# Performance work log

Measured on AMD Instinct MI355X. Metric: run time of the kernel, lower is better.

## Reference

```python
import jax, jax.numpy as jnp
import numpy as np

POOL = 7                     # cfg.POOLING_SIZE
PRE = 2 * POOL               # pre_pool_size (max_pool=True path)
LEVEL_HW = (256, 128, 64, 32)  # square H=W of P2..P5 for a 1024x1024 image


def setup_inputs() -> dict:
    key = jax.random.key(0)
    ks = jax.random.split(key, 8)
    C = 256
    feats = {f"p{i + 2}": jax.random.normal(ks[i], (1, C, s, s), dtype=jnp.float32)
             for i, s in enumerate(LEVEL_HW)}
    N = 1000
    IMG = 1024.0
    x1 = jax.random.uniform(ks[4], (N,), minval=0.0, maxval=IMG - 33.0)
    y1 = jax.random.uniform(ks[5], (N,), minval=0.0, maxval=IMG - 33.0)
    w = jax.random.uniform(ks[6], (N,), minval=32.0, maxval=512.0)
    h = jax.random.uniform(ks[7], (N,), minval=32.0, maxval=512.0)
    x2 = jnp.minimum(x1 + w, IMG - 1.0)
    y2 = jnp.minimum(y1 + h, IMG - 1.0)
    rois = jnp.stack([jnp.zeros((N,), jnp.float32), x1, y1, x2, y2], axis=1)
    inp = dict(feats)
    inp["rois"] = rois
    return inp


def _crop_pool_fpn(p2, p3, p4, p5, rois):
    """Faithful vectorized version of Network._crop_pool_layer_fpn (max_pool=True).

    Per-ROI FPN level select, affine-grid + bilinear grid_sample
    (align_corners=True semantics, zeros padding), then 2x2 max pool.
    """
    levels = (p2, p3, p4, p5)
    C = p2.shape[1]
    Hm = p2.shape[2]  # largest (P2) map; all levels padded up to this
    # Pad every level into one [L, Hm, Wm, C] array (NHWC for clean gathers).
    feats = jnp.stack([
        jnp.pad(jnp.transpose(f[0], (1, 2, 0)),
                ((0, Hm - f.shape[2]), (0, Hm - f.shape[3]), (0, 0)))
        for f in levels])

    x1, y1, x2, y2 = rois[:, 1], rois[:, 2], rois[:, 3], rois[:, 4]
    w = jnp.where(x2 - x1 <= 0, 1e-14, x2 - x1)
    h = jnp.where(y2 - y1 <= 0, 1e-14, y2 - y1)
    kf = 4.0 + jnp.log2(jnp.sqrt(w * h) / 224.0)   # k0 + log2(sqrt(wh)/224)
    kf = jnp.clip(kf, 2.0, 5.0)                     # clamp BEFORE round (as in source)
    k = jnp.round(kf)
    scale = 2.0 ** k
    lvl = k.astype(jnp.int32) - 2                   # [N] in [0,4)
    x1s, y1s, x2s, y2s = x1 / scale, y1 / scale, x2 / scale, y2 / scale

    # affine_grid(theta) + align_corners=True grid_sample collapses to direct
    # pixel coords: px = (x1+x2)/2 + t*(x2-x1)/2, t = linspace(-1, 1, PRE).
    t = jnp.linspace(-1.0, 1.0, PRE)
    px = (x1s + x2s)[:, None] * 0.5 + t[None, :] * ((x2s - x1s)[:, None] * 0.5)  # [N,PRE]
    py = (y1s + y2s)[:, None] * 0.5 + t[None, :] * ((y2s - y1s)[:, None] * 0.5)
    PX = jnp.broadcast_to(px[:, None, :], (px.shape[0], PRE, PRE))  # [N,PRE,PRE]
    PY = jnp.broadcast_to(py[:, :, None], (py.shape[0], PRE, PRE))

    HWl = jnp.asarray(LEVEL_HW, jnp.float32)[lvl][:, None, None]  # per-ROI level size (square)
    x0 = jnp.floor(PX)
    y0 = jnp.floor(PY)
    dx = PX - x0
    dy = PY - y0

    def gather(yi, xi):
        inb = ((xi >= 0) & (xi < HWl) & (yi >= 0) & (yi < HWl)).astype(feats.dtype)
        yc = jnp.clip(yi, 0, Hm - 1).astype(jnp.int32)
        xc = jnp.clip(xi, 0, Hm - 1).astype(jnp.int32)
        v = feats[lvl[:, None, None], yc, xc]      # [N,PRE,PRE,C]
        return v * inb[..., None]                   # zeros padding

    out = (gather(y0, x0) * ((1 - dy) * (1 - dx))[..., None]
           + gather(y0, x0 + 1) * ((1 - dy) * dx)[..., None]
           + gather(y0 + 1, x0) * (dy * (1 - dx))[..., None]
           + gather(y0 + 1, x0 + 1) * (dy * dx)[..., None])  # [N,PRE,PRE,C]

    crops = jnp.transpose(out, (0, 3, 1, 2))        # [N,C,PRE,PRE]
    N = crops.shape[0]
    crops = crops.reshape(N, C, POOL, 2, POOL, 2).max(axis=(3, 5))  # 2x2 max pool
    return crops                                     # [N,C,POOL,POOL]


def reference(p2, p3, p4, p5, rois):
    return _crop_pool_fpn(p2, p3, p4, p5, rois)
```

## Files before the change

### kernel.cpp

```cpp
#include <hip/hip_runtime.h>
#include <math.h>

#define C_CH 256
#define PRE 14
#define NPOOL 7
#define PIX (NPOOL * NPOOL)
#define OUT_PER_ROI (C_CH * PIX)
#define HALF_OUT (128 * PIX)
#define SROW 132

#define OFF_P2 0
#define OFF_P3 16777216u
#define OFF_P4 20971520u
#define OFF_P5 22020096u
#define WS_ELEMS 22282240u

#define RB 528
#define NTRANS 680
#define NBKT 4096

static __device__ __forceinline__ unsigned short f2bf(float f) {
    unsigned int u = __float_as_uint(f);
    unsigned int r = (u + 0x7FFFu + ((u >> 16) & 1u)) >> 16;
    return (unsigned short)r;
}
static __device__ __forceinline__ float bfLO(unsigned int u) { return __uint_as_float(u << 16); }
static __device__ __forceinline__ float bfHI(unsigned int u) { return __uint_as_float(u & 0xFFFF0000u); }

static __device__ __forceinline__ void bilerp8(uint4 a00, uint4 a01, uint4 a10, uint4 a11,
                                               float4 w, float4& lo, float4& hi) {
    lo.x = fmaf(bfLO(a00.x), w.x, fmaf(bfLO(a01.x), w.y, fmaf(bfLO(a10.x), w.z, bfLO(a11.x) * w.w)));
    lo.y = fmaf(bfHI(a00.x), w.x, fmaf(bfHI(a01.x), w.y, fmaf(bfHI(a10.x), w.z, bfHI(a11.x) * w.w)));
    lo.z = fmaf(bfLO(a00.y), w.x, fmaf(bfLO(a01.y), w.y, fmaf(bfLO(a10.y), w.z, bfLO(a11.y) * w.w)));
    lo.w = fmaf(bfHI(a00.y), w.x, fmaf(bfHI(a01.y), w.y, fmaf(bfHI(a10.y), w.z, bfHI(a11.y) * w.w)));
    hi.x = fmaf(bfLO(a00.z), w.x, fmaf(bfLO(a01.z), w.y, fmaf(bfLO(a10.z), w.z, bfLO(a11.z) * w.w)));
    hi.y = fmaf(bfHI(a00.z), w.x, fmaf(bfHI(a01.z), w.y, fmaf(bfHI(a10.z), w.z, bfHI(a11.z) * w.w)));
    hi.z = fmaf(bfLO(a00.w), w.x, fmaf(bfLO(a01.w), w.y, fmaf(bfLO(a10.w), w.z, bfLO(a11.w) * w.w)));
    hi.w = fmaf(bfHI(a00.w), w.x, fmaf(bfHI(a01.w), w.y, fmaf(bfHI(a10.w), w.z, bfHI(a11.w) * w.w)));
}

__global__ __launch_bounds__(256) void transpose_all_k(
    const float* __restrict__ p2, const float* __restrict__ p3,
    const float* __restrict__ p4, const float* __restrict__ p5,
    unsigned short* __restrict__ ws, const float* __restrict__ rois,
    unsigned* __restrict__ perm, int N) {
    __shared__ unsigned char lds[128 * RB];

    if (blockIdx.x == 0) {
        int* hist = (int*)lds;
        int* tsum = (int*)(lds + NBKT * 4);
        unsigned short* kbuf = (unsigned short*)(lds + NBKT * 4 + 1024);
        const int t = threadIdx.x;
        #pragma unroll
        for (int k = 0; k < NBKT / 256; ++k) hist[t + (k << 8)] = 0;
        __syncthreads();
        for (int i = t; i < N; i += 256) {
            const float x1 = rois[i * 5 + 1];
            const float y1 = rois[i * 5 + 2];
            const float x2 = rois[i * 5 + 3];
            const float y2 = rois[i * 5 + 4];
            float w = x2 - x1; w = (w <= 0.f) ? 1e-14f : w;
            float h = y2 - y1; h = (h <= 0.f) ? 1e-14f : h;
            float kf = 4.f + log2f(sqrtf(w * h) * (1.f / 224.f));
            kf = fminf(fmaxf(kf, 2.f), 5.f);
            const float kr = rintf(kf);
            const int lvl = (int)kr - 2;
            const float inv = exp2f(-kr);
            const int yi = (int)(y1 * inv);
            const int xi = (int)(x1 * inv);
            const int sh = 3 - lvl;
            const int yb = (yi >> sh) & 31;
            const int xb = (xi >> sh) & 31;
            const int bkt = (lvl << 10) | (yb << 5) | xb;
            kbuf[i] = (unsigned short)bkt;
            atomicAdd(&hist[bkt], 1);
        }
        __syncthreads();
        {
            const int b0 = t << 4;
            int s = 0;
            #pragma unroll
            for (int k = 0; k < 16; ++k) s += hist[b0 + k];
            tsum[t] = s;
        }
        __syncthreads();
        if (t == 0) {
            int acc = 0;
            for (int k = 0; k < 256; ++k) { const int v = tsum[k]; tsum[k] = acc; acc += v; }
        }
        __syncthreads();
        {
            const int b0 = t << 4;
            int run = tsum[t];
            #pragma unroll
            for (int k = 0; k < 16; ++k) { const int v = hist[b0 + k]; hist[b0 + k] = run; run += v; }
        }
        __syncthreads();
        for (int i = t; i < N; i += 256) {
            const int pos = atomicAdd(&hist[kbuf[i]], 1);
            perm[pos] = (unsigned)i;
        }
        return;
    }

    int b = blockIdx.x - 1;
    const float* __restrict__ src;
    int HW2; unsigned int off;
    if (b < 512)      { src = p2; HW2 = 65536; off = OFF_P2; }
    else if (b < 640) { src = p3; HW2 = 16384; off = OFF_P3; b -= 512; }
    else if (b < 672) { src = p4; HW2 = 4096;  off = OFF_P4; b -= 640; }
    else              { src = p5; HW2 = 1024;  off = OFF_P5; b -= 672; }
    const int hw0 = b << 7;

    const int t   = threadIdx.x;
    const int hwq = t & 31;
    const int cg  = t >> 5;
    const int key = (hwq & 7) << 4;

    #pragma unroll
    for (int s = 0; s < 8; ++s) {
        const int c0 = (cg << 2) + (s << 5);
        const float* g = src + (size_t)c0 * HW2 + hw0 + (hwq << 2);
        const float4 a0 = *(const float4*)(g);
        const float4 a1 = *(const float4*)(g + HW2);
        const float4 a2 = *(const float4*)(g + 2 * (size_t)HW2);
        const float4 a3 = *(const float4*)(g + 3 * (size_t)HW2);
        const int cb = (c0 << 1) ^ key;
        unsigned char* base = &lds[(hwq << 2) * RB + cb];
        ushort4 w;
        w.x = f2bf(a0.x); w.y = f2bf(a1.x); w.z = f2bf(a2.x); w.w = f2bf(a3.x);
        *(ushort4*)(base) = w;
        w.x = f2bf(a0.y); w.y = f2bf(a1.y); w.z = f2bf(a2.y); w.w = f2bf(a3.y);
        *(ushort4*)(base + RB) = w;
        w.x = f2bf(a0.z); w.y = f2bf(a1.z); w.z = f2bf(a2.z); w.w = f2bf(a3.z);
        *(ushort4*)(base + 2 * RB) = w;
        w.x = f2bf(a0.w); w.y = f2bf(a1.w); w.z = f2bf(a2.w); w.w = f2bf(a3.w);
        *(ushort4*)(base + 3 * RB) = w;
    }
    __syncthreads();

    char* __restrict__ dstb = (char*)(ws + off + ((size_t)hw0 << 8));
    const int chunk = t & 31;
    const int hwl   = t >> 5;
    #pragma unroll
    for (int p = 0; p < 16; ++p) {
        const int hw = (p << 3) + hwl;
        const int k2 = ((hw >> 2) & 7) << 4;
        const uint4 v = *(const uint4*)&lds[hw * RB + ((chunk << 4) ^ k2)];
        *(uint4*)(dstb + hw * 512 + (chunk << 4)) = v;
    }
}

template <bool HWC>
__global__ __launch_bounds__(256, 4) void roi_align_k(
    const float* __restrict__ p2, const float* __restrict__ p3,
    const float* __restrict__ p4, const float* __restrict__ p5,
    const unsigned short* __restrict__ ws, const float* __restrict__ rois,
    const unsigned* __restrict__ perm, int N, float* __restrict__ out) {

    __shared__ float sxw0[PRE], sxw1[PRE], syw0[PRE], syw1[PRE];
    __shared__ int   sxc0[PRE], sxc1[PRE], syc0[PRE], syc1[PRE];
    __shared__ float4 wtab[PRE * PRE];
    __shared__ int4   otab[PRE * PRE];
    __shared__ float  sout[PIX * SROW];

    int n;
    if (HWC) {
        const int bid = blockIdx.x;
        int spos;
        if ((N & 7) == 0) spos = (bid & 7) * (N >> 3) + (bid >> 3);
        else              spos = bid;
        n = (int)perm[spos];
    } else {
        n = blockIdx.x;
    }
    const int ch0 = blockIdx.y << 7;
    const float x1 = rois[n * 5 + 1];
    const float y1 = rois[n * 5 + 2];
    const float x2 = rois[n * 5 + 3];
    const float y2 = rois[n * 5 + 4];

    float w = x2 - x1; w = (w <= 0.f) ? 1e-14f : w;
    float h = y2 - y1; h = (h <= 0.f) ? 1e-14f : h;
    float kf = 4.f + log2f(sqrtf(w * h) * (1.f / 224.f));
    kf = fminf(fmaxf(kf, 2.f), 5.f);
    const float kr = rintf(kf);
    const int   lvl = (int)kr - 2;
    const float scale = exp2f(kr);
    const int   HW = 256 >> lvl;

    const int t = threadIdx.x;

    if (t < 2 * PRE) {
        const bool isx = t < PRE;
        const int  j = isx ? t : t - PRE;
        const float a1 = isx ? x1 : y1;
        const float a2 = isx ? x2 : y2;
        const float a1s = a1 / scale, a2s = a2 / scale;
        const float cen  = (a1s + a2s) * 0.5f;
        const float half = (a2s - a1s) * 0.5f;
        const float tt = -1.f + (2.f / 13.f) * (float)j;
        const float p  = cen + tt * half;
        const float p0 = floorf(p);
        const float d  = p - p0;
        const float HWf = (float)HW;
        const float m0 = (p0 >= 0.f && p0 < HWf) ? 1.f : 0.f;
        const float m1 = (p0 + 1.f >= 0.f && p0 + 1.f < HWf) ? 1.f : 0.f;
        const int c0i = min(max((int)p0, 0), HW - 1);
        const int c1i = min(max((int)p0 + 1, 0), HW - 1);
        if (isx) { sxw0[j] = (1.f - d) * m0; sxw1[j] = d * m1; sxc0[j] = c0i; sxc1[j] = c1i; }
        else     { syw0[j] = (1.f - d) * m0; syw1[j] = d * m1; syc0[j] = c0i; syc1[j] = c1i; }
    }
    __syncthreads();

    if (HWC) {
        for (int s = t; s < PRE * PRE; s += 256) {
            const int i = s / PRE;
            const int j = s - i * PRE;
            wtab[s] = make_float4(syw0[i] * sxw0[j], syw0[i] * sxw1[j],
                                  syw1[i] * sxw0[j], syw1[i] * sxw1[j]);
            otab[s] = make_int4((syc0[i] * HW + sxc0[j]) << 9, (syc0[i] * HW + sxc1[j]) << 9,
                                (syc1[i] * HW + sxc0[j]) << 9, (syc1[i] * HW + sxc1[j]) << 9);
        }
        __syncthreads();
    }

    if (HWC) {
        const int g   = t & 15;
        const int ph  = t >> 4;
        const unsigned int off = (lvl == 0) ? OFF_P2 : (lvl == 1) ? OFF_P3 : (lvl == 2) ? OFF_P4 : OFF_P5;
        const char* __restrict__ base = (const char*)(ws + off);
        const int cb2 = (ch0 + (g << 3)) << 1;

        #define DO_PIXEL(P)                                                           \
        {                                                                             \
            const int p_ = (P);                                                       \
            const int oy_ = p_ / 7;                                                   \
            const int ox_ = p_ - oy_ * 7;                                             \
            const int s00 = oy_ * 28 + (ox_ << 1);                                    \
            const int4  oA = otab[s00];      const float4 wA = wtab[s00];             \
            const int4  oB = otab[s00 + 1];  const float4 wB = wtab[s00 + 1];         \
            const int4  oC = otab[s00 + 14]; const float4 wC = wtab[s00 + 14];        \
            const int4  oD = otab[s00 + 15]; const float4 wD = wtab[s00 + 15];        \
            const uint4 A00 = *(const uint4*)(base + (oA.x + cb2));                   \
            const uint4 A01 = *(const uint4*)(base + (oA.y + cb2));                   \
            const uint4 A10 = *(const uint4*)(base + (oA.z + cb2));                   \
            const uint4 A11 = *(const uint4*)(base + (oA.w + cb2));                   \
            const uint4 B00 = *(const uint4*)(base + (oB.x + cb2));                   \
            const uint4 B01 = *(const uint4*)(base + (oB.y + cb2));                   \
            const uint4 B10 = *(const uint4*)(base + (oB.z + cb2));                   \
            const uint4 B11 = *(const uint4*)(base + (oB.w + cb2));                   \
            const uint4 C00 = *(const uint4*)(base + (oC.x + cb2));                   \
            const uint4 C01 = *(const uint4*)(base + (oC.y + cb2));                   \
            const uint4 C10 = *(const uint4*)(base + (oC.z + cb2));                   \
            const uint4 C11 = *(const uint4*)(base + (oC.w + cb2));                   \
            const uint4 D00 = *(const uint4*)(base + (oD.x + cb2));                   \
            const uint4 D01 = *(const uint4*)(base + (oD.y + cb2));                   \
            const uint4 D10 = *(const uint4*)(base + (oD.z + cb2));                   \
            const uint4 D11 = *(const uint4*)(base + (oD.w + cb2));                   \
            float4 aLo, aHi, bLo, bHi, cLo, cHi, dLo, dHi;                            \
            bilerp8(A00, A01, A10, A11, wA, aLo, aHi);                                \
            bilerp8(B00, B01, B10, B11, wB, bLo, bHi);                                \
            bilerp8(C00, C01, C10, C11, wC, cLo, cHi);                                \
            bilerp8(D00, D01, D10, D11, wD, dLo, dHi);                                \
            float4 mLo, mHi;                                                          \
            mLo.x = fmaxf(fmaxf(aLo.x, bLo.x), fmaxf(cLo.x, dLo.x));                  \
            mLo.y = fmaxf(fmaxf(aLo.y, bLo.y), fmaxf(cLo.y, dLo.y));                  \
            mLo.z = fmaxf(fmaxf(aLo.z, bLo.z), fmaxf(cLo.z, dLo.z));                  \
            mLo.w = fmaxf(fmaxf(aLo.w, bLo.w), fmaxf(cLo.w, dLo.w));                  \
            mHi.x = fmaxf(fmaxf(aHi.x, bHi.x), fmaxf(cHi.x, dHi.x));                  \
            mHi.y = fmaxf(fmaxf(aHi.y, bHi.y), fmaxf(cHi.y, dHi.y));                  \
            mHi.z = fmaxf(fmaxf(aHi.z, bHi.z), fmaxf(cHi.z, dHi.z));                  \
            mHi.w = fmaxf(fmaxf(aHi.w, bHi.w), fmaxf(cHi.w, dHi.w));                  \
            *(float4*)&sout[p_ * SROW + (g << 3)] = mLo;                              \
            *(float4*)&sout[p_ * SROW + (g << 3) + 4] = mHi;                          \
        }

        DO_PIXEL(ph)
        DO_PIXEL(ph + 16)
        DO_PIXEL(ph + 32)
        if (ph == 0) DO_PIXEL(48)
        #undef DO_PIXEL
    } else {
        const int g     = t & 31;
        const int s     = t >> 5;
        const int cbase = ch0 + (g << 2);
        const float* __restrict__ fbF = (lvl == 0) ? p2 : (lvl == 1) ? p3 : (lvl == 2) ? p4 : p5;
        const int HW2 = HW * HW;
        for (int p = s; p < PIX; p += 8) {
            const int oy = p / 7;
            const int ox = p - oy * 7;
            float4 m = make_float4(-3.4e38f, -3.4e38f, -3.4e38f, -3.4e38f);
            #pragma unroll
            for (int sy = 0; sy < 2; ++sy) {
                const int i = oy * 2 + sy;
                const float wy0 = syw0[i], wy1 = syw1[i];
                const int   yc0 = syc0[i], yc1 = syc1[i];
                #pragma unroll
                for (int sx = 0; sx < 2; ++sx) {
                    const int j = ox * 2 + sx;
                    const float w00 = wy0 * sxw0[j], w01 = wy0 * sxw1[j];
                    const float w10 = wy1 * sxw0[j], w11 = wy1 * sxw1[j];
                    const int   xc0 = sxc0[j], xc1 = sxc1[j];
                    float vv[4];
                    #pragma unroll
                    for (int k = 0; k < 4; ++k) {
                        const size_t cb = (size_t)(cbase + k) * HW2;
                        const float a00 = fbF[cb + yc0 * HW + xc0];
                        const float a01 = fbF[cb + yc0 * HW + xc1];
                        const float a10 = fbF[cb + yc1 * HW + xc0];
                        const float a11 = fbF[cb + yc1 * HW + xc1];
                        vv[k] = fmaf(a00, w00, fmaf(a01, w01, fmaf(a10, w10, a11 * w11)));
                    }
                    m.x = fmaxf(m.x, vv[0]);
                    m.y = fmaxf(m.y, vv[1]);
                    m.z = fmaxf(m.z, vv[2]);
                    m.w = fmaxf(m.w, vv[3]);
                }
            }
            *(float4*)&sout[p * SROW + (g << 2)] = m;
        }
    }
    __syncthreads();

    const size_t ob = (size_t)n * OUT_PER_ROI + (size_t)ch0 * PIX;
    for (int o = t; o < HALF_OUT; o += 256) {
        const int c  = o / PIX;
        const int pp = o - c * PIX;
        out[ob + o] = sout[pp * SROW + c];
    }
}

extern "C" void kernel_launch(void* const* d_in, const int* in_sizes, int n_in,
                              void* d_out, int out_size, void* d_ws, size_t ws_size,
                              hipStream_t stream) {
    const float* p2   = (const float*)d_in[0];
    const float* p3   = (const float*)d_in[1];
    const float* p4   = (const float*)d_in[2];
    const float* p5   = (const float*)d_in[3];
    const float* rois = (const float*)d_in[4];
    float* out = (float*)d_out;
    const int N = in_sizes[4] / 5;

    const size_t need = (size_t)WS_ELEMS * sizeof(unsigned short) + 4096;
    if (ws_size >= need && N <= 1024) {
        unsigned short* ws = (unsigned short*)d_ws;
        unsigned* perm = (unsigned*)((char*)d_ws + (size_t)WS_ELEMS * sizeof(unsigned short));
        transpose_all_k<<<NTRANS + 1, 256, 0, stream>>>(p2, p3, p4, p5, ws, rois, perm, N);
        roi_align_k<true><<<dim3(N, 2), 256, 0, stream>>>(p2, p3, p4, p5, ws, rois, perm, N, out);
    } else {
        roi_align_k<false><<<dim3(N, 2), 256, 0, stream>>>(p2, p3, p4, p5, nullptr, rois, nullptr, N, out);
    }
}
```

Measured before the change: 48.85 us.

## Walk pooled rows per warp-slot and reuse neighbouring bilinear taps across columns

Replaces the per-pixel gather of 16 independent uint4 taps with a per-output-row loop in which each of 7 slots sweeps the 14 sample columns serially, caching the two most recent column taps and skipping reloads when column or row indices coincide. Each thread now handles 4 channels (uint2 loads) instead of 8, and the LDS weight/offset tables and their extra barrier are removed. The aim is fewer redundant global loads when ROIs are upsampled from small feature regions. In exchange, only 7 of 8 wave slots do work, the column loop is serial with unroll 1 and data-dependent branches, so memory-level parallelism per thread drops.

```diff
diff --git a/kernel.cpp b/kernel.cpp
--- a/kernel.cpp
+++ b/kernel.cpp
@@ -27,16 +27,17 @@
 static __device__ __forceinline__ float bfLO(unsigned int u) { return __uint_as_float(u << 16); }
 static __device__ __forceinline__ float bfHI(unsigned int u) { return __uint_as_float(u & 0xFFFF0000u); }
 
-static __device__ __forceinline__ void bilerp8(uint4 a00, uint4 a01, uint4 a10, uint4 a11,
-                                               float4 w, float4& lo, float4& hi) {
-    lo.x = fmaf(bfLO(a00.x), w.x, fmaf(bfLO(a01.x), w.y, fmaf(bfLO(a10.x), w.z, bfLO(a11.x) * w.w)));
-    lo.y = fmaf(bfHI(a00.x), w.x, fmaf(bfHI(a01.x), w.y, fmaf(bfHI(a10.x), w.z, bfHI(a11.x) * w.w)));
-    lo.z = fmaf(bfLO(a00.y), w.x, fmaf(bfLO(a01.y), w.y, fmaf(bfLO(a10.y), w.z, bfLO(a11.y) * w.w)));
-    lo.w = fmaf(bfHI(a00.y), w.x, fmaf(bfHI(a01.y), w.y, fmaf(bfHI(a10.y), w.z, bfHI(a11.y) * w.w)));
-    hi.x = fmaf(bfLO(a00.z), w.x, fmaf(bfLO(a01.z), w.y, fmaf(bfLO(a10.z), w.z, bfLO(a11.z) * w.w)));
-    hi.y = fmaf(bfHI(a00.z), w.x, fmaf(bfHI(a01.z), w.y, fmaf(bfHI(a10.z), w.z, bfHI(a11.z) * w.w)));
-    hi.z = fmaf(bfLO(a00.w), w.x, fmaf(bfLO(a01.w), w.y, fmaf(bfLO(a10.w), w.z, bfLO(a11.w) * w.w)));
-    hi.w = fmaf(bfHI(a00.w), w.x, fmaf(bfHI(a01.w), w.y, fmaf(bfHI(a10.w), w.z, bfHI(a11.w) * w.w)));
+static __device__ __forceinline__ float4 bf4(uint2 u) {
+    return make_float4(bfLO(u.x), bfHI(u.x), bfLO(u.y), bfHI(u.y));
+}
+static __device__ __forceinline__ float4 fma4(float4 a, float s, float4 c) {
+    return make_float4(fmaf(a.x, s, c.x), fmaf(a.y, s, c.y), fmaf(a.z, s, c.z), fmaf(a.w, s, c.w));
+}
+static __device__ __forceinline__ float4 mul4(float4 a, float s) {
+    return make_float4(a.x * s, a.y * s, a.z * s, a.w * s);
+}
+static __device__ __forceinline__ float4 max4(float4 a, float4 b) {
+    return make_float4(fmaxf(a.x, b.x), fmaxf(a.y, b.y), fmaxf(a.z, b.z), fmaxf(a.w, b.w));
 }
 
 __global__ __launch_bounds__(256) void transpose_all_k(
@@ -160,9 +161,7 @@
 
     __shared__ float sxw0[PRE], sxw1[PRE], syw0[PRE], syw1[PRE];
     __shared__ int   sxc0[PRE], sxc1[PRE], syc0[PRE], syc1[PRE];
-    __shared__ float4 wtab[PRE * PRE];
-    __shared__ int4   otab[PRE * PRE];
-    __shared__ float  sout[PIX * SROW];
+    __shared__ float sout[PIX * SROW];
 
     int n;
     if (HWC) {
@@ -213,81 +212,78 @@
     }
     __syncthreads();
 
+    const int g    = t & 31;
+    const int slot = t >> 5;
+
     if (HWC) {
-        for (int s = t; s < PRE * PRE; s += 256) {
-            const int i = s / PRE;
-            const int j = s - i * PRE;
-            wtab[s] = make_float4(syw0[i] * sxw0[j], syw0[i] * sxw1[j],
-                                  syw1[i] * sxw0[j], syw1[i] * sxw1[j]);
-            otab[s] = make_int4((syc0[i] * HW + sxc0[j]) << 9, (syc0[i] * HW + sxc1[j]) << 9,
-                                (syc1[i] * HW + sxc0[j]) << 9, (syc1[i] * HW + sxc1[j]) << 9);
-        }
-        __syncthreads();
-    }
-
-    if (HWC) {
-        const int g   = t & 15;
-        const int ph  = t >> 4;
         const unsigned int off = (lvl == 0) ? OFF_P2 : (lvl == 1) ? OFF_P3 : (lvl == 2) ? OFF_P4 : OFF_P5;
-        const char* __restrict__ base = (const char*)(ws + off);
-        const int cb2 = (ch0 + (g << 3)) << 1;
-
-        #define DO_PIXEL(P)                                                           \
-        {                                                                             \
-            const int p_ = (P);                                                       \
-            const int oy_ = p_ / 7;                                                   \
-            const int ox_ = p_ - oy_ * 7;                                             \
-            const int s00 = oy_ * 28 + (ox_ << 1);                                    \
-            const int4  oA = otab[s00];      const float4 wA = wtab[s00];             \
-            const int4  oB = otab[s00 + 1];  const float4 wB = wtab[s00 + 1];         \
-            const int4  oC = otab[s00 + 14]; const float4 wC = wtab[s00 + 14];        \
-            const int4  oD = otab[s00 + 15]; const float4 wD = wtab[s00 + 15];        \
-            const uint4 A00 = *(const uint4*)(base + (oA.x + cb2));                   \
-            const uint4 A01 = *(const uint4*)(base + (oA.y + cb2));                   \
-            const uint4 A10 = *(const uint4*)(base + (oA.z + cb2));                   \
-            const uint4 A11 = *(const uint4*)(base + (oA.w + cb2));                   \
-            const uint4 B00 = *(const uint4*)(base + (oB.x + cb2));                   \
-            const uint4 B01 = *(const uint4*)(base + (oB.y + cb2));                   \
-            const uint4 B10 = *(const uint4*)(base + (oB.z + cb2));                   \
-            const uint4 B11 = *(const uint4*)(base + (oB.w + cb2));                   \
-            const uint4 C00 = *(const uint4*)(base + (oC.x + cb2));                   \
-            const uint4 C01 = *(const uint4*)(base + (oC.y + cb2));                   \
-            const uint4 C10 = *(const uint4*)(base + (oC.z + cb2));                   \
-            const uint4 C11 = *(const uint4*)(base + (oC.w + cb2));                   \
-            const uint4 D00 = *(const uint4*)(base + (oD.x + cb2));                   \
-            const uint4 D01 = *(const uint4*)(base + (oD.y + cb2));                   \
-            const uint4 D10 = *(const uint4*)(base + (oD.z + cb2));                   \
-            const uint4 D11 = *(const uint4*)(base + (oD.w + cb2));                   \
-            float4 aLo, aHi, bLo, bHi, cLo, cHi, dLo, dHi;                            \
-            bilerp8(A00, A01, A10, A11, wA, aLo, aHi);                                \
-            bilerp8(B00, B01, B10, B11, wB, bLo, bHi);                                \
-            bilerp8(C00, C01, C10, C11, wC, cLo, cHi);                                \
-            bilerp8(D00, D01, D10, D11, wD, dLo, dHi);                                \
-            float4 mLo, mHi;                                                          \
-            mLo.x = fmaxf(fmaxf(aLo.x, bLo.x), fmaxf(cLo.x, dLo.x));                  \
-            mLo.y = fmaxf(fmaxf(aLo.y, bLo.y), fmaxf(cLo.y, dLo.y));                  \
-            mLo.z = fmaxf(fmaxf(aLo.z, bLo.z), fmaxf(cLo.z, dLo.z));                  \
-            mLo.w = fmaxf(fmaxf(aLo.w, bLo.w), fmaxf(cLo.w, dLo.w));                  \
-            mHi.x = fmaxf(fmaxf(aHi.x, bHi.x), fmaxf(cHi.x, dHi.x));                  \
-            mHi.y = fmaxf(fmaxf(aHi.y, bHi.y), fmaxf(cHi.y, dHi.y));                  \
-            mHi.z = fmaxf(fmaxf(aHi.z, bHi.z), fmaxf(cHi.z, dHi.z));                  \
-            mHi.w = fmaxf(fmaxf(aHi.w, bHi.w), fmaxf(cHi.w, dHi.w));                  \
-            *(float4*)&sout[p_ * SROW + (g << 3)] = mLo;                              \
-            *(float4*)&sout[p_ * SROW + (g << 3) + 4] = mHi;                          \
-        }
-
-        DO_PIXEL(ph)
-        DO_PIXEL(ph + 16)
-        DO_PIXEL(ph + 32)
-        if (ph == 0) DO_PIXEL(48)
-        #undef DO_PIXEL
+        const char* __restrict__ base = (const char*)(ws + off) + ((ch0 + (g << 2)) << 1);
+
+        if (slot < NPOOL) {
+            const int oy = slot;
+            const int i0 = oy << 1, i1 = i0 + 1;
+            const int R0 = syc0[i0], R1 = syc1[i0], R2 = syc0[i1], R3 = syc1[i1];
+            const float wy0 = syw0[i0], wy1 = syw1[i0], wy2 = syw0[i1], wy3 = syw1[i1];
+            const int rb0 = (R0 * HW) << 9;
+            const int rb1 = (R1 * HW) << 9;
+            const int rb2 = (R2 * HW) << 9;
+            const int rb3 = (R3 * HW) << 9;
+
+            int xA = -1, xB = -1;
+            uint2 A0, A1, A2, A3, B0, B1, B2, B3;
+            float4 pprev = make_float4(0.f, 0.f, 0.f, 0.f);
+
+            #pragma unroll 1
+            for (int j = 0; j < PRE; ++j) {
+                const int a = sxc0[j], b = sxc1[j];
+                const float wxa = sxw0[j], wxb = sxw1[j];
+                uint2 Ca0, Ca1, Ca2, Ca3, Cb0, Cb1, Cb2, Cb3;
+
+                if (a == xA)      { Ca0 = A0; Ca1 = A1; Ca2 = A2; Ca3 = A3; }
+                else if (a == xB) { Ca0 = B0; Ca1 = B1; Ca2 = B2; Ca3 = B3; }
+                else {
+                    const int xo = a << 9;
+                    Ca0 = *(const uint2*)(base + (rb0 + xo));
+                    if (R1 == R0) Ca1 = Ca0; else Ca1 = *(const uint2*)(base + (rb1 + xo));
+                    if (R2 == R1) Ca2 = Ca1; else if (R2 == R0) Ca2 = Ca0;
+                    else Ca2 = *(const uint2*)(base + (rb2 + xo));
+                    if (R3 == R2) Ca3 = Ca2; else Ca3 = *(const uint2*)(base + (rb3 + xo));
+                }
+                if (b == a)       { Cb0 = Ca0; Cb1 = Ca1; Cb2 = Ca2; Cb3 = Ca3; }
+                else if (b == xB) { Cb0 = B0; Cb1 = B1; Cb2 = B2; Cb3 = B3; }
+                else if (b == xA) { Cb0 = A0; Cb1 = A1; Cb2 = A2; Cb3 = A3; }
+                else {
+                    const int xo = b << 9;
+                    Cb0 = *(const uint2*)(base + (rb0 + xo));
+                    if (R1 == R0) Cb1 = Cb0; else Cb1 = *(const uint2*)(base + (rb1 + xo));
+                    if (R2 == R1) Cb2 = Cb1; else if (R2 == R0) Cb2 = Cb0;
+                    else Cb2 = *(const uint2*)(base + (rb2 + xo));
+                    if (R3 == R2) Cb3 = Cb2; else Cb3 = *(const uint2*)(base + (rb3 + xo));
+                }
+                xA = a; A0 = Ca0; A1 = Ca1; A2 = Ca2; A3 = Ca3;
+                xB = b; B0 = Cb0; B1 = Cb1; B2 = Cb2; B3 = Cb3;
+
+                float4 ta = fma4(bf4(Ca1), wy1, mul4(bf4(Ca0), wy0));
+                float4 tb = fma4(bf4(Cb1), wy1, mul4(bf4(Cb0), wy0));
+                const float4 v0 = fma4(tb, wxb, mul4(ta, wxa));
+                ta = fma4(bf4(Ca3), wy3, mul4(bf4(Ca2), wy2));
+                tb = fma4(bf4(Cb3), wy3, mul4(bf4(Cb2), wy2));
+                const float4 v1 = fma4(tb, wxb, mul4(ta, wxa));
+                const float4 vj = max4(v0, v1);
+
+                if ((j & 1) == 0) {
+                    pprev = vj;
+                } else {
+                    const float4 o = max4(pprev, vj);
+                    *(float4*)&sout[(oy * 7 + (j >> 1)) * SROW + (g << 2)] = o;
+                }
+            }
+        }
     } else {
-        const int g     = t & 31;
-        const int s     = t >> 5;
         const int cbase = ch0 + (g << 2);
         const float* __restrict__ fbF = (lvl == 0) ? p2 : (lvl == 1) ? p3 : (lvl == 2) ? p4 : p5;
         const int HW2 = HW * HW;
-        for (int p = s; p < PIX; p += 8) {
+        for (int p = slot; p < PIX; p += 8) {
             const int oy = p / 7;
             const int ox = p - oy * 7;
             float4 m = make_float4(-3.4e38f, -3.4e38f, -3.4e38f, -3.4e38f);
```

After: 75.20 us. 53.9% more time.
